# Performance work log

Measured on AMD Instinct MI355X. Metric: run time of the kernel, lower is better.

## Reference

```python
import jax, jax.numpy as jnp
import numpy as np

N, E, F_IN, H, C = 50000, 800000, 256, 4, 32
NEG_SLOPE_ATT = 0.2   # PyG GATConv default negative_slope for attention LeakyReLU
NEG_SLOPE_ACT = 0.01  # GATLayer's alpha for the post-norm LeakyReLU
EPS = 1e-5            # BatchNorm1d eps


def setup_inputs() -> dict:
    key = jax.random.key(0)
    ks = jax.random.split(key, 8)
    x = jax.random.normal(ks[0], (N, F_IN), jnp.float32)
    edge_idx = jax.random.randint(ks[1], (2, E), 0, N)
    # GATConv params (heads concatenated): lin weight, attention vectors, bias
    W = jax.random.normal(ks[2], (H * C, F_IN), jnp.float32) / np.sqrt(F_IN)
    att_src = jax.random.normal(ks[3], (H, C), jnp.float32) / np.sqrt(C)
    att_dst = jax.random.normal(ks[4], (H, C), jnp.float32) / np.sqrt(C)
    bias = jax.random.normal(ks[5], (H * C,), jnp.float32) * 0.01
    # BatchNorm1d affine params
    gamma = jax.random.normal(ks[6], (H * C,), jnp.float32) * 0.1 + 1.0
    beta = jax.random.normal(ks[7], (H * C,), jnp.float32) * 0.01
    return {"x": x, "edge_idx": edge_idx, "W": W, "att_src": att_src,
            "att_dst": att_dst, "bias": bias, "gamma": gamma, "beta": beta}


def reference(x, edge_idx, W, att_src, att_dst, bias, gamma, beta):
    n = x.shape[0]
    # PyG GATConv adds self-loops by default
    self_loops = jnp.arange(n)
    src = jnp.concatenate([edge_idx[0], self_loops])  # [E+N]
    dst = jnp.concatenate([edge_idx[1], self_loops])

    h = (x @ W.T).reshape(n, H, C)                    # [N, H, C]
    a_s = jnp.einsum('nhc,hc->nh', h, att_src)        # per-node src score
    a_d = jnp.einsum('nhc,hc->nh', h, att_dst)        # per-node dst score

    # edge attention logits, then segment softmax over incoming edges per dst
    e = jax.nn.leaky_relu(a_s[src] + a_d[dst], NEG_SLOPE_ATT)  # [E+N, H]
    e_max = jax.ops.segment_max(e, dst, num_segments=n)
    e_exp = jnp.exp(e - e_max[dst])
    denom = jax.ops.segment_sum(e_exp, dst, num_segments=n)
    alpha = e_exp / denom[dst]                        # [E+N, H]

    # scatter-add aggregation of attended source features
    out = jax.ops.segment_sum(alpha[:, :, None] * h[src], dst, num_segments=n)
    out = out.reshape(n, H * C) + bias                # concat heads + bias

    # BatchNorm1d (training-mode batch statistics) + LeakyReLU(alpha)
    mu = out.mean(axis=0)
    var = out.var(axis=0)
    out = (out - mu) * jax.lax.rsqrt(var + EPS) * gamma + beta
    return jax.nn.leaky_relu(out, NEG_SLOPE_ACT)
```

## Files before the change

### kernel.cpp

```cpp
#include <hip/hip_runtime.h>
#include <hip/hip_bf16.h>
#include <math.h>


typedef __attribute__((ext_vector_type(8))) short bf8_t;
typedef __attribute__((ext_vector_type(4))) float f4_t;

__device__ inline unsigned short f2bf(float f) {
  unsigned u = __float_as_uint(f);
  u += 0x7fff + ((u >> 16) & 1);
  return (unsigned short)(u >> 16);
}
__device__ inline float lrelu02(float v) { return v > 0.f ? v : 0.2f * v; }
__device__ inline float bflo(unsigned g) { return __uint_as_float(g << 16); }
__device__ inline float bfhi(unsigned g) { return __uint_as_float(g & 0xffff0000u); }

#define LSTRIDE 264
#define PSTRIDE 2048
#define SSTRIDE 2112
#define NC 32

__global__ __launch_bounds__(256) void gemm_mfma(const float* __restrict__ x,
                                                 const float* __restrict__ w,
                                                 const float* __restrict__ att_s,
                                                 const float* __restrict__ att_d,
                                                 unsigned* __restrict__ hb2,
                                                 float* __restrict__ a_s,
                                                 float* __restrict__ a_d,
                                                 int n, int ntiles) {
  __shared__ unsigned short wsl[128 * LSTRIDE];
  __shared__ unsigned short xsl[64 * LSTRIDE];
  int tid = threadIdx.x;
  int lane = tid & 63;
  int wid = tid >> 6;
  int quad = lane >> 4;
  int l15 = lane & 15;

  float attS[8], attD[8];
#pragma unroll
  for (int t = 0; t < 8; t++) {
    attS[t] = att_s[t * 16 + l15];
    attD[t] = att_d[t * 16 + l15];
  }

#pragma unroll 4
  for (int i = 0; i < 32; i++) {
    int idx = tid + i * 256;
    int row = idx >> 6;
    int f4 = idx & 63;
    float4 v = *(const float4*)&w[(size_t)row * 256 + f4 * 4];
    unsigned p01 = f2bf(v.x) | ((unsigned)f2bf(v.y) << 16);
    unsigned p23 = f2bf(v.z) | ((unsigned)f2bf(v.w) << 16);
    *(uint2*)&wsl[row * LSTRIDE + f4 * 4] = make_uint2(p01, p23);
  }

  float4 pre[16];
  int tile = blockIdx.x;
  if (tile < ntiles) {
#pragma unroll
    for (int i = 0; i < 16; i++) {
      int idx = tid + i * 256;
      int row = idx >> 6, f4 = idx & 63;
      int grow = tile * 64 + row;
      pre[i] = (grow < n) ? *(const float4*)&x[(size_t)grow * 256 + f4 * 4]
                          : make_float4(0.f, 0.f, 0.f, 0.f);
    }
  }

  for (; tile < ntiles; tile += gridDim.x) {
    __syncthreads();
#pragma unroll
    for (int i = 0; i < 16; i++) {
      int idx = tid + i * 256;
      int row = idx >> 6, f4 = idx & 63;
      unsigned p01 = f2bf(pre[i].x) | ((unsigned)f2bf(pre[i].y) << 16);
      unsigned p23 = f2bf(pre[i].z) | ((unsigned)f2bf(pre[i].w) << 16);
      *(uint2*)&xsl[row * LSTRIDE + f4 * 4] = make_uint2(p01, p23);
    }
    __syncthreads();

    int nxt = tile + gridDim.x;
    if (nxt < ntiles) {
#pragma unroll
      for (int i = 0; i < 16; i++) {
        int idx = tid + i * 256;
        int row = idx >> 6, f4 = idx & 63;
        int grow = nxt * 64 + row;
        pre[i] = (grow < n) ? *(const float4*)&x[(size_t)grow * 256 + f4 * 4]
                            : make_float4(0.f, 0.f, 0.f, 0.f);
      }
    }

    f4_t acc[8];
#pragma unroll
    for (int t = 0; t < 8; t++) acc[t] = (f4_t){0.f, 0.f, 0.f, 0.f};
    const unsigned short* arow = &xsl[(wid * 16 + l15) * LSTRIDE];
#pragma unroll
    for (int ks = 0; ks < 8; ks++) {
      bf8_t af = *(const bf8_t*)&arow[ks * 32 + quad * 8];
#pragma unroll
      for (int t = 0; t < 8; t++) {
        bf8_t bf = *(const bf8_t*)&wsl[(t * 16 + l15) * LSTRIDE + ks * 32 + quad * 8];
        acc[t] = __builtin_amdgcn_mfma_f32_16x16x32_bf16(af, bf, acc[t], 0, 0, 0);
      }
    }

    int growb = tile * 64 + wid * 16 + quad * 4;
#pragma unroll
    for (int r = 0; r < 4; r++) {
      int grow = growb + r;
      bool ok = grow < n;
      if (ok) {
        unsigned* orow = &hb2[(size_t)grow * 64];
#pragma unroll
        for (int t = 0; t < 4; t++)
          orow[t * 16 + l15] =
              (unsigned)f2bf(acc[t][r]) | ((unsigned)f2bf(acc[t + 4][r]) << 16);
      }
      float sp[4], dp[4];
#pragma unroll
      for (int hh = 0; hh < 4; hh++) {
        sp[hh] = acc[2 * hh][r] * attS[2 * hh] + acc[2 * hh + 1][r] * attS[2 * hh + 1];
        dp[hh] = acc[2 * hh][r] * attD[2 * hh] + acc[2 * hh + 1][r] * attD[2 * hh + 1];
      }
#pragma unroll
      for (int mm = 1; mm < 16; mm <<= 1) {
#pragma unroll
        for (int hh = 0; hh < 4; hh++) {
          sp[hh] += __shfl_xor(sp[hh], mm, 64);
          dp[hh] += __shfl_xor(dp[hh], mm, 64);
        }
      }
      float vs = l15 == 0 ? sp[0] : l15 == 1 ? sp[1] : l15 == 2 ? sp[2] : sp[3];
      float vd = l15 == 0 ? dp[0] : l15 == 1 ? dp[1] : l15 == 2 ? dp[2] : dp[3];
      if (ok && l15 < 4) {
        a_s[grow * 4 + l15] = vs;
        a_d[grow * 4 + l15] = vd;
      }
    }
  }
}

__global__ __launch_bounds__(1024) void pair_scatter3_k(const int* __restrict__ src,
                                                        const int* __restrict__ dst,
                                                        int* __restrict__ bcnt,
                                                        unsigned* __restrict__ pairs,
                                                        int E, int nb) {
  __shared__ int cnt[1024];
  int t = threadIdx.x;
  int chunk = (E + gridDim.x - 1) / gridDim.x;
  int lo = blockIdx.x * chunk;
  int hi = min(E, lo + chunk);
  for (int i = t; i < nb; i += 1024) cnt[i] = 0;
  __syncthreads();
  for (int i = lo + t; i < hi; i += 1024) atomicAdd(&cnt[dst[i] >> 6], 1);
  __syncthreads();
  for (int i = t; i < nb; i += 1024) {
    int c = cnt[i];
    cnt[i] = c ? atomicAdd(&bcnt[i], c) : 0;
  }
  __syncthreads();
  for (int i = lo + t; i < hi; i += 1024) {
    int d = dst[i];
    int b = d >> 6;
    int pos = atomicAdd(&cnt[b], 1);
    if (pos < PSTRIDE)
      pairs[(size_t)b * PSTRIDE + pos] = (unsigned)src[i] | ((unsigned)(d & 63) << 26);
  }
}

__global__ __launch_bounds__(256) void bucket_csr_k(const unsigned* __restrict__ pairs,
                                                    const int* __restrict__ bcnt,
                                                    int* __restrict__ off,
                                                    int* __restrict__ dlen,
                                                    int* __restrict__ ssrc, int n) {
  __shared__ int hist[64], lofs[64], curs[64];
  int b = blockIdx.x;
  int t = threadIdx.x;
  int d0 = b << 6;
  int dcnt = min(64, n - d0);
  int cnt = min(bcnt[b], PSTRIDE);
  size_t pstart = (size_t)b * PSTRIDE;
  int ob = b * SSTRIDE;
  if (t < 64) hist[t] = (t < dcnt) ? 1 : 0;
  __syncthreads();
  for (int i = t; i < cnt; i += 256) atomicAdd(&hist[pairs[pstart + i] >> 26], 1);
  __syncthreads();
  if (t == 0) {
    int acc = 0;
    for (int k = 0; k < 64; k++) { lofs[k] = acc; acc += hist[k]; }
  }
  __syncthreads();
  if (t < dcnt) {
    int lo = lofs[t];
    off[d0 + t] = ob + lo;
    dlen[d0 + t] = hist[t];
    curs[t] = lo + 1;
    ssrc[ob + lo] = d0 + t;
  }
  __syncthreads();
  for (int i = t; i < cnt; i += 256) {
    unsigned u = pairs[pstart + i];
    int dl = u >> 26;
    int pos = ob + atomicAdd(&curs[dl], 1);
    ssrc[pos] = (int)(u & 0x03FFFFFFu);
  }
}

#define FMA4(g, p)                                                            \
  alo0 = fmaf(p.x, bflo(g.x), alo0); ahi0 = fmaf(p.y, bfhi(g.x), ahi0);       \
  alo1 = fmaf(p.x, bflo(g.y), alo1); ahi1 = fmaf(p.y, bfhi(g.y), ahi1);       \
  alo2 = fmaf(p.x, bflo(g.z), alo2); ahi2 = fmaf(p.y, bfhi(g.z), ahi2);       \
  alo3 = fmaf(p.x, bflo(g.w), alo3); ahi3 = fmaf(p.y, bfhi(g.w), ahi3);

__global__ __launch_bounds__(256) void agg_csr_k(const int* __restrict__ off,
                                                 const int* __restrict__ dlen,
                                                 const int* __restrict__ ssrc,
                                                 const float* __restrict__ a_s,
                                                 const float* __restrict__ a_d,
                                                 const unsigned* __restrict__ hb2,
                                                 float* __restrict__ out,
                                                 float* __restrict__ gstat, int n) {
  __shared__ float lp[4][64 * 4];
  __shared__ int lsrc[4][64];
  __shared__ float bstat[4][256];
  int tid = threadIdx.x;
  int wid = tid >> 6;
  int lane = tid & 63;
  int d = blockIdx.x * 4 + wid;
  bool act = d < n;
  int q = lane >> 4;
  int m = lane & 15;
  int hsel = m >> 3;

  float alo0 = 0.f, alo1 = 0.f, alo2 = 0.f, alo3 = 0.f;
  float ahi0 = 0.f, ahi1 = 0.f, ahi2 = 0.f, ahi3 = 0.f;
  float l0 = 0.f, l1 = 0.f, l2 = 0.f, l3 = 0.f;

  if (act) {
    int start = off[d];
    int end = start + dlen[d];
    float4 ad4 = *(const float4*)&a_d[d * 4];
    for (int base = start; base < end; base += 64) {
      int cnt = min(64, end - base);
      int j = base + lane;
      if (j < end) {
        int s = ssrc[j];
        float4 as4 = *(const float4*)&a_s[s * 4];
        float p0 = __expf(lrelu02(as4.x + ad4.x));
        float p1 = __expf(lrelu02(as4.y + ad4.y));
        float p2 = __expf(lrelu02(as4.z + ad4.z));
        float p3 = __expf(lrelu02(as4.w + ad4.w));
        l0 += p0; l1 += p1; l2 += p2; l3 += p3;
        lsrc[wid][lane] = s;
        *(float4*)&lp[wid][lane * 4] = make_float4(p0, p2, p1, p3);
      }
      int k = 0;
      for (; k + 8 <= cnt; k += 8) {
        int e0 = k + q, e1 = k + 4 + q;
        int s0 = lsrc[wid][e0], s1 = lsrc[wid][e1];
        uint4 g0 = *(const uint4*)&hb2[(size_t)s0 * 64 + m * 4];
        uint4 g1 = *(const uint4*)&hb2[(size_t)s1 * 64 + m * 4];
        float2 p0 = *(const float2*)&lp[wid][e0 * 4 + hsel * 2];
        float2 p1 = *(const float2*)&lp[wid][e1 * 4 + hsel * 2];
        FMA4(g0, p0);
        FMA4(g1, p1);
      }
      for (; k + 4 <= cnt; k += 4) {
        int e0 = k + q;
        int s0 = lsrc[wid][e0];
        uint4 g0 = *(const uint4*)&hb2[(size_t)s0 * 64 + m * 4];
        float2 p0 = *(const float2*)&lp[wid][e0 * 4 + hsel * 2];
        FMA4(g0, p0);
      }
      int rem = cnt - k;
      if (q < rem) {
        int e0 = k + q;
        int s0 = lsrc[wid][e0];
        uint4 g0 = *(const uint4*)&hb2[(size_t)s0 * 64 + m * 4];
        float2 p0 = *(const float2*)&lp[wid][e0 * 4 + hsel * 2];
        FMA4(g0, p0);
      }
    }
  }

#pragma unroll
  for (int o = 16; o < 64; o <<= 1) {
    alo0 += __shfl_xor(alo0, o, 64); alo1 += __shfl_xor(alo1, o, 64);
    alo2 += __shfl_xor(alo2, o, 64); alo3 += __shfl_xor(alo3, o, 64);
    ahi0 += __shfl_xor(ahi0, o, 64); ahi1 += __shfl_xor(ahi1, o, 64);
    ahi2 += __shfl_xor(ahi2, o, 64); ahi3 += __shfl_xor(ahi3, o, 64);
  }
#pragma unroll
  for (int o = 1; o < 64; o <<= 1) {
    l0 += __shfl_xor(l0, o, 64);
    l1 += __shfl_xor(l1, o, 64);
    l2 += __shfl_xor(l2, o, 64);
    l3 += __shfl_xor(l3, o, 64);
  }
  float il_lo = 1.0f / (hsel ? l1 : l0);
  float il_hi = 1.0f / (hsel ? l3 : l2);
  float4 flo = make_float4(0.f, 0.f, 0.f, 0.f);
  float4 fhi = make_float4(0.f, 0.f, 0.f, 0.f);
  if (act) {
    flo = make_float4(alo0 * il_lo, alo1 * il_lo, alo2 * il_lo, alo3 * il_lo);
    fhi = make_float4(ahi0 * il_hi, ahi1 * il_hi, ahi2 * il_hi, ahi3 * il_hi);
  }
  if (q == 0) {
    if (act) {
      *(float4*)&out[(size_t)d * 128 + m * 4] = flo;
      *(float4*)&out[(size_t)d * 128 + 64 + m * 4] = fhi;
    }
    *(float4*)&bstat[wid][m * 4] = flo;
    *(float4*)&bstat[wid][64 + m * 4] = fhi;
    *(float4*)&bstat[wid][128 + m * 4] =
        make_float4(flo.x * flo.x, flo.y * flo.y, flo.z * flo.z, flo.w * flo.w);
    *(float4*)&bstat[wid][192 + m * 4] =
        make_float4(fhi.x * fhi.x, fhi.y * fhi.y, fhi.z * fhi.z, fhi.w * fhi.w);
  }
  __syncthreads();
  float v = bstat[0][tid] + bstat[1][tid] + bstat[2][tid] + bstat[3][tid];
  atomicAdd(&gstat[(blockIdx.x & (NC - 1)) * 256 + tid], v);
}

__global__ __launch_bounds__(256) void bn_apply_k(float* __restrict__ out,
                                                  const float* __restrict__ gstat,
                                                  const float* __restrict__ gamma,
                                                  const float* __restrict__ beta,
                                                  float inv_n, int n4) {
  __shared__ float sc[128], sh[128];
  int tid = threadIdx.x;
  if (tid < 128) {
    float s = 0.f, s2 = 0.f;
#pragma unroll 8
    for (int c = 0; c < NC; c++) {
      s += gstat[c * 256 + tid];
      s2 += gstat[c * 256 + 128 + tid];
    }
    float mu = s * inv_n;
    float var = s2 * inv_n - mu * mu;
    float rstd = 1.0f / sqrtf(var + 1e-5f);
    float g = gamma[tid] * rstd;
    sc[tid] = g;
    sh[tid] = beta[tid] - mu * g;
  }
  __syncthreads();
  int i = blockIdx.x * 256 + tid;
  if (i >= n4) return;
  float4 v = ((float4*)out)[i];
  int j = (i & 31) << 2;
  const float4 scv = *(const float4*)&sc[j];
  const float4 shv = *(const float4*)&sh[j];
  v.x = fmaf(v.x, scv.x, shv.x);
  v.y = fmaf(v.y, scv.y, shv.y);
  v.z = fmaf(v.z, scv.z, shv.z);
  v.w = fmaf(v.w, scv.w, shv.w);
  v.x = v.x > 0.f ? v.x : 0.01f * v.x;
  v.y = v.y > 0.f ? v.y : 0.01f * v.y;
  v.z = v.z > 0.f ? v.z : 0.01f * v.z;
  v.w = v.w > 0.f ? v.w : 0.01f * v.w;
  ((float4*)out)[i] = v;
}

static inline char* align16(char* p) {
  return (char*)(((uintptr_t)p + 15) & ~(uintptr_t)15);
}

extern "C" void kernel_launch(void* const* d_in, const int* in_sizes, int n_in,
                              void* d_out, int out_size, void* d_ws, size_t ws_size,
                              hipStream_t stream) {
  const float* x     = (const float*)d_in[0];
  const int*   ei    = (const int*)d_in[1];
  const float* W     = (const float*)d_in[2];
  const float* att_s = (const float*)d_in[3];
  const float* att_d = (const float*)d_in[4];
  const float* gamma = (const float*)d_in[6];
  const float* beta  = (const float*)d_in[7];

  int n = in_sizes[0] / 256;
  int E = in_sizes[1] / 2;
  const int* src = ei;
  const int* dstp = ei + E;
  float* out = (float*)d_out;

  int NBUCK = (n + 63) >> 6;
  int ntiles = (n + 63) / 64;

  char* p = (char*)d_ws;
  unsigned* hb2 = (unsigned*)p; p = align16(p + (size_t)n * 64 * 4);
  float* a_s   = (float*)p; p = align16(p + (size_t)n * 4 * 4);
  float* a_d   = (float*)p; p = align16(p + (size_t)n * 4 * 4);
  float* gstat = (float*)p;
  int*   bcnt  = (int*)(gstat + NC * 256);
  p = align16((char*)(bcnt + NBUCK));
  int* off     = (int*)p;   p = align16(p + (size_t)n * 4);
  int* dlen    = (int*)p;   p = align16(p + (size_t)n * 4);
  int* ssrc    = (int*)p;   p = align16(p + (size_t)NBUCK * SSTRIDE * 4);
  unsigned* pairs = (unsigned*)p; p = align16(p + (size_t)NBUCK * PSTRIDE * 4);

  hipMemsetAsync(gstat, 0, ((size_t)NC * 256 + NBUCK) * 4, stream);

  gemm_mfma<<<256, 256, 0, stream>>>(x, W, att_s, att_d, hb2, a_s, a_d, n, ntiles);

  pair_scatter3_k<<<64, 1024, 0, stream>>>(src, dstp, bcnt, pairs, E, NBUCK);
  bucket_csr_k<<<NBUCK, 256, 0, stream>>>(pairs, bcnt, off, dlen, ssrc, n);

  agg_csr_k<<<(n + 3) / 4, 256, 0, stream>>>(off, dlen, ssrc, a_s, a_d, hb2, out,
                                             gstat, n);

  bn_apply_k<<<(n * 32 + 255) / 256, 256, 0, stream>>>(out, gstat, gamma, beta,
                                                       1.0f / n, n * 32);
}
```

Before: 206.2 us.

## Process four destination nodes per wave in aggregation and unroll gathers by 16

The aggregation kernel now has each wave loop over DPW=4 destination nodes. BN partial statistics are accumulated in shared memory across those nodes before a single atomicAdd per block, which cuts the block count and global atomic traffic by about 4x. The number of stat copies (NC) drops from 32 to 8, and a 16-edge unrolled gather loop adds memory-level parallelism. The costs are fewer blocks in flight, serialized per-node work within a wave, and more atomic contention on fewer slots.

```diff
diff --git a/kernel.cpp b/kernel.cpp
--- a/kernel.cpp
+++ b/kernel.cpp
@@ -18,7 +18,8 @@
 #define LSTRIDE 264
 #define PSTRIDE 2048
 #define SSTRIDE 2112
-#define NC 32
+#define NC 8
+#define DPW 4
 
 __global__ __launch_bounds__(256) void gemm_mfma(const float* __restrict__ x,
                                                  const float* __restrict__ w,
@@ -227,17 +228,22 @@
   int tid = threadIdx.x;
   int wid = tid >> 6;
   int lane = tid & 63;
-  int d = blockIdx.x * 4 + wid;
-  bool act = d < n;
   int q = lane >> 4;
   int m = lane & 15;
   int hsel = m >> 3;
-
-  float alo0 = 0.f, alo1 = 0.f, alo2 = 0.f, alo3 = 0.f;
-  float ahi0 = 0.f, ahi1 = 0.f, ahi2 = 0.f, ahi3 = 0.f;
-  float l0 = 0.f, l1 = 0.f, l2 = 0.f, l3 = 0.f;
-
-  if (act) {
+  const unsigned* __restrict__ hb2m = hb2 + m * 4;
+
+  *(float4*)&bstat[wid][lane * 4] = make_float4(0.f, 0.f, 0.f, 0.f);
+
+  int dbase = (blockIdx.x * 4 + wid) * DPW;
+  for (int it = 0; it < DPW; it++) {
+    int d = dbase + it;
+    if (d >= n) break;
+
+    float alo0 = 0.f, alo1 = 0.f, alo2 = 0.f, alo3 = 0.f;
+    float ahi0 = 0.f, ahi1 = 0.f, ahi2 = 0.f, ahi3 = 0.f;
+    float l0 = 0.f, l1 = 0.f, l2 = 0.f, l3 = 0.f;
+
     int start = off[d];
     int end = start + dlen[d];
     float4 ad4 = *(const float4*)&a_d[d * 4];
@@ -256,11 +262,28 @@
         *(float4*)&lp[wid][lane * 4] = make_float4(p0, p2, p1, p3);
       }
       int k = 0;
+      for (; k + 16 <= cnt; k += 16) {
+        int e0 = k + q, e1 = k + 4 + q, e2 = k + 8 + q, e3 = k + 12 + q;
+        int s0 = lsrc[wid][e0], s1 = lsrc[wid][e1];
+        int s2 = lsrc[wid][e2], s3 = lsrc[wid][e3];
+        uint4 g0 = *(const uint4*)&hb2m[(size_t)s0 * 64];
+        uint4 g1 = *(const uint4*)&hb2m[(size_t)s1 * 64];
+        uint4 g2 = *(const uint4*)&hb2m[(size_t)s2 * 64];
+        uint4 g3 = *(const uint4*)&hb2m[(size_t)s3 * 64];
+        float2 p0 = *(const float2*)&lp[wid][e0 * 4 + hsel * 2];
+        float2 p1 = *(const float2*)&lp[wid][e1 * 4 + hsel * 2];
+        float2 p2 = *(const float2*)&lp[wid][e2 * 4 + hsel * 2];
+        float2 p3 = *(const float2*)&lp[wid][e3 * 4 + hsel * 2];
+        FMA4(g0, p0);
+        FMA4(g1, p1);
+        FMA4(g2, p2);
+        FMA4(g3, p3);
+      }
       for (; k + 8 <= cnt; k += 8) {
         int e0 = k + q, e1 = k + 4 + q;
         int s0 = lsrc[wid][e0], s1 = lsrc[wid][e1];
-        uint4 g0 = *(const uint4*)&hb2[(size_t)s0 * 64 + m * 4];
-        uint4 g1 = *(const uint4*)&hb2[(size_t)s1 * 64 + m * 4];
+        uint4 g0 = *(const uint4*)&hb2m[(size_t)s0 * 64];
+        uint4 g1 = *(const uint4*)&hb2m[(size_t)s1 * 64];
         float2 p0 = *(const float2*)&lp[wid][e0 * 4 + hsel * 2];
         float2 p1 = *(const float2*)&lp[wid][e1 * 4 + hsel * 2];
         FMA4(g0, p0);
@@ -269,7 +292,7 @@
       for (; k + 4 <= cnt; k += 4) {
         int e0 = k + q;
         int s0 = lsrc[wid][e0];
-        uint4 g0 = *(const uint4*)&hb2[(size_t)s0 * 64 + m * 4];
+        uint4 g0 = *(const uint4*)&hb2m[(size_t)s0 * 64];
         float2 p0 = *(const float2*)&lp[wid][e0 * 4 + hsel * 2];
         FMA4(g0, p0);
       }
@@ -277,47 +300,50 @@
       if (q < rem) {
         int e0 = k + q;
         int s0 = lsrc[wid][e0];
-        uint4 g0 = *(const uint4*)&hb2[(size_t)s0 * 64 + m * 4];
+        uint4 g0 = *(const uint4*)&hb2m[(size_t)s0 * 64];
         float2 p0 = *(const float2*)&lp[wid][e0 * 4 + hsel * 2];
         FMA4(g0, p0);
       }
     }
-  }
-
-#pragma unroll
-  for (int o = 16; o < 64; o <<= 1) {
-    alo0 += __shfl_xor(alo0, o, 64); alo1 += __shfl_xor(alo1, o, 64);
-    alo2 += __shfl_xor(alo2, o, 64); alo3 += __shfl_xor(alo3, o, 64);
-    ahi0 += __shfl_xor(ahi0, o, 64); ahi1 += __shfl_xor(ahi1, o, 64);
-    ahi2 += __shfl_xor(ahi2, o, 64); ahi3 += __shfl_xor(ahi3, o, 64);
-  }
-#pragma unroll
-  for (int o = 1; o < 64; o <<= 1) {
-    l0 += __shfl_xor(l0, o, 64);
-    l1 += __shfl_xor(l1, o, 64);
-    l2 += __shfl_xor(l2, o, 64);
-    l3 += __shfl_xor(l3, o, 64);
-  }
-  float il_lo = 1.0f / (hsel ? l1 : l0);
-  float il_hi = 1.0f / (hsel ? l3 : l2);
-  float4 flo = make_float4(0.f, 0.f, 0.f, 0.f);
-  float4 fhi = make_float4(0.f, 0.f, 0.f, 0.f);
-  if (act) {
-    flo = make_float4(alo0 * il_lo, alo1 * il_lo, alo2 * il_lo, alo3 * il_lo);
-    fhi = make_float4(ahi0 * il_hi, ahi1 * il_hi, ahi2 * il_hi, ahi3 * il_hi);
-  }
-  if (q == 0) {
-    if (act) {
+
+#pragma unroll
+    for (int o = 16; o < 64; o <<= 1) {
+      alo0 += __shfl_xor(alo0, o, 64); alo1 += __shfl_xor(alo1, o, 64);
+      alo2 += __shfl_xor(alo2, o, 64); alo3 += __shfl_xor(alo3, o, 64);
+      ahi0 += __shfl_xor(ahi0, o, 64); ahi1 += __shfl_xor(ahi1, o, 64);
+      ahi2 += __shfl_xor(ahi2, o, 64); ahi3 += __shfl_xor(ahi3, o, 64);
+    }
+#pragma unroll
+    for (int o = 1; o < 64; o <<= 1) {
+      l0 += __shfl_xor(l0, o, 64);
+      l1 += __shfl_xor(l1, o, 64);
+      l2 += __shfl_xor(l2, o, 64);
+      l3 += __shfl_xor(l3, o, 64);
+    }
+    float il_lo = 1.0f / (hsel ? l1 : l0);
+    float il_hi = 1.0f / (hsel ? l3 : l2);
+    if (q == 0) {
+      float4 flo = make_float4(alo0 * il_lo, alo1 * il_lo, alo2 * il_lo, alo3 * il_lo);
+      float4 fhi = make_float4(ahi0 * il_hi, ahi1 * il_hi, ahi2 * il_hi, ahi3 * il_hi);
       *(float4*)&out[(size_t)d * 128 + m * 4] = flo;
       *(float4*)&out[(size_t)d * 128 + 64 + m * 4] = fhi;
-    }
-    *(float4*)&bstat[wid][m * 4] = flo;
-    *(float4*)&bstat[wid][64 + m * 4] = fhi;
-    *(float4*)&bstat[wid][128 + m * 4] =
-        make_float4(flo.x * flo.x, flo.y * flo.y, flo.z * flo.z, flo.w * flo.w);
-    *(float4*)&bstat[wid][192 + m * 4] =
-        make_float4(fhi.x * fhi.x, fhi.y * fhi.y, fhi.z * fhi.z, fhi.w * fhi.w);
-  }
+      float4 b0 = *(float4*)&bstat[wid][m * 4];
+      b0.x += flo.x; b0.y += flo.y; b0.z += flo.z; b0.w += flo.w;
+      *(float4*)&bstat[wid][m * 4] = b0;
+      float4 b1 = *(float4*)&bstat[wid][64 + m * 4];
+      b1.x += fhi.x; b1.y += fhi.y; b1.z += fhi.z; b1.w += fhi.w;
+      *(float4*)&bstat[wid][64 + m * 4] = b1;
+      float4 b2 = *(float4*)&bstat[wid][128 + m * 4];
+      b2.x += flo.x * flo.x; b2.y += flo.y * flo.y;
+      b2.z += flo.z * flo.z; b2.w += flo.w * flo.w;
+      *(float4*)&bstat[wid][128 + m * 4] = b2;
+      float4 b3 = *(float4*)&bstat[wid][192 + m * 4];
+      b3.x += fhi.x * fhi.x; b3.y += fhi.y * fhi.y;
+      b3.z += fhi.z * fhi.z; b3.w += fhi.w * fhi.w;
+      *(float4*)&bstat[wid][192 + m * 4] = b3;
+    }
+  }
+
   __syncthreads();
   float v = bstat[0][tid] + bstat[1][tid] + bstat[2][tid] + bstat[3][tid];
   atomicAdd(&gstat[(blockIdx.x & (NC - 1)) * 256 + tid], v);
@@ -332,7 +358,7 @@
   int tid = threadIdx.x;
   if (tid < 128) {
     float s = 0.f, s2 = 0.f;
-#pragma unroll 8
+#pragma unroll
     for (int c = 0; c < NC; c++) {
       s += gstat[c * 256 + tid];
       s2 += gstat[c * 256 + 128 + tid];
@@ -405,8 +431,9 @@
   pair_scatter3_k<<<64, 1024, 0, stream>>>(src, dstp, bcnt, pairs, E, NBUCK);
   bucket_csr_k<<<NBUCK, 256, 0, stream>>>(pairs, bcnt, off, dlen, ssrc, n);
 
-  agg_csr_k<<<(n + 3) / 4, 256, 0, stream>>>(off, dlen, ssrc, a_s, a_d, hb2, out,
-                                             gstat, n);
+  agg_csr_k<<<(n + 4 * DPW - 1) / (4 * DPW), 256, 0, stream>>>(off, dlen, ssrc,
+                                                               a_s, a_d, hb2, out,
+                                                               gstat, n);
 
   bn_apply_k<<<(n * 32 + 255) / 256, 256, 0, stream>>>(out, gstat, gamma, beta,
                                                        1.0f / n, n * 32);
```

Result: no change. 206.8 us (+0.3%).

## Fold attention vectors into GEMM weights and unroll CSR aggregation gather by 16

Applied to the files above, without the earlier changes.

Precomputes att·W as eight extra weight rows, stored as hi/lo bf16 pairs, so the MFMA GEMM produces the a_s/a_d scores directly as a ninth output tile. This replaces the per-row dot products and 16-lane shuffle reductions. The aggregation loop gains a 16-edge unrolled stage so more independent gathers are in flight, and the BN stat partition count drops from 32 to 8. In exchange it adds a small extra kernel launch, an extra MFMA tile per k-step, and more contention on the stat atomics.

```diff
diff --git a/kernel.cpp b/kernel.cpp
--- a/kernel.cpp
+++ b/kernel.cpp
@@ -18,30 +18,37 @@
 #define LSTRIDE 264
 #define PSTRIDE 2048
 #define SSTRIDE 2112
-#define NC 32
+#define NC 8
+
+__global__ __launch_bounds__(256) void att_fold_k(const float* __restrict__ w,
+                                                  const float* __restrict__ att_s,
+                                                  const float* __restrict__ att_d,
+                                                  float* __restrict__ waug) {
+  int j = blockIdx.x;
+  int head = j & 3;
+  const float* av = (j < 4 ? att_s : att_d) + head * 32;
+  int col = threadIdx.x;
+  float s = 0.f;
+#pragma unroll
+  for (int c = 0; c < 32; c++)
+    s += av[c] * w[(size_t)(head * 32 + c) * 256 + col];
+  waug[j * 256 + col] = s;
+}
 
 __global__ __launch_bounds__(256) void gemm_mfma(const float* __restrict__ x,
                                                  const float* __restrict__ w,
-                                                 const float* __restrict__ att_s,
-                                                 const float* __restrict__ att_d,
+                                                 const float* __restrict__ waug,
                                                  unsigned* __restrict__ hb2,
                                                  float* __restrict__ a_s,
                                                  float* __restrict__ a_d,
                                                  int n, int ntiles) {
-  __shared__ unsigned short wsl[128 * LSTRIDE];
+  __shared__ unsigned short wsl[144 * LSTRIDE];
   __shared__ unsigned short xsl[64 * LSTRIDE];
   int tid = threadIdx.x;
   int lane = tid & 63;
   int wid = tid >> 6;
   int quad = lane >> 4;
   int l15 = lane & 15;
-
-  float attS[8], attD[8];
-#pragma unroll
-  for (int t = 0; t < 8; t++) {
-    attS[t] = att_s[t * 16 + l15];
-    attD[t] = att_d[t * 16 + l15];
-  }
 
 #pragma unroll 4
   for (int i = 0; i < 32; i++) {
@@ -53,6 +60,17 @@
     unsigned p23 = f2bf(v.z) | ((unsigned)f2bf(v.w) << 16);
     *(uint2*)&wsl[row * LSTRIDE + f4 * 4] = make_uint2(p01, p23);
   }
+#pragma unroll
+  for (int i = 0; i < 8; i++) {
+    int idx = tid + i * 256;
+    int row = idx >> 8;
+    int col = idx & 255;
+    float v = waug[idx];
+    unsigned short hi = f2bf(v);
+    float lov = v - __uint_as_float((unsigned)hi << 16);
+    wsl[(128 + row) * LSTRIDE + col] = hi;
+    wsl[(136 + row) * LSTRIDE + col] = f2bf(lov);
+  }
 
   float4 pre[16];
   int tile = blockIdx.x;
@@ -91,15 +109,15 @@
       }
     }
 
-    f4_t acc[8];
-#pragma unroll
-    for (int t = 0; t < 8; t++) acc[t] = (f4_t){0.f, 0.f, 0.f, 0.f};
+    f4_t acc[9];
+#pragma unroll
+    for (int t = 0; t < 9; t++) acc[t] = (f4_t){0.f, 0.f, 0.f, 0.f};
     const unsigned short* arow = &xsl[(wid * 16 + l15) * LSTRIDE];
 #pragma unroll
     for (int ks = 0; ks < 8; ks++) {
       bf8_t af = *(const bf8_t*)&arow[ks * 32 + quad * 8];
 #pragma unroll
-      for (int t = 0; t < 8; t++) {
+      for (int t = 0; t < 9; t++) {
         bf8_t bf = *(const bf8_t*)&wsl[(t * 16 + l15) * LSTRIDE + ks * 32 + quad * 8];
         acc[t] = __builtin_amdgcn_mfma_f32_16x16x32_bf16(af, bf, acc[t], 0, 0, 0);
       }
@@ -117,25 +135,11 @@
           orow[t * 16 + l15] =
               (unsigned)f2bf(acc[t][r]) | ((unsigned)f2bf(acc[t + 4][r]) << 16);
       }
-      float sp[4], dp[4];
-#pragma unroll
-      for (int hh = 0; hh < 4; hh++) {
-        sp[hh] = acc[2 * hh][r] * attS[2 * hh] + acc[2 * hh + 1][r] * attS[2 * hh + 1];
-        dp[hh] = acc[2 * hh][r] * attD[2 * hh] + acc[2 * hh + 1][r] * attD[2 * hh + 1];
-      }
-#pragma unroll
-      for (int mm = 1; mm < 16; mm <<= 1) {
-#pragma unroll
-        for (int hh = 0; hh < 4; hh++) {
-          sp[hh] += __shfl_xor(sp[hh], mm, 64);
-          dp[hh] += __shfl_xor(dp[hh], mm, 64);
-        }
-      }
-      float vs = l15 == 0 ? sp[0] : l15 == 1 ? sp[1] : l15 == 2 ? sp[2] : sp[3];
-      float vd = l15 == 0 ? dp[0] : l15 == 1 ? dp[1] : l15 == 2 ? dp[2] : dp[3];
-      if (ok && l15 < 4) {
-        a_s[grow * 4 + l15] = vs;
-        a_d[grow * 4 + l15] = vd;
+      float v8 = acc[8][r];
+      v8 += __shfl_xor(v8, 8, 64);
+      if (ok) {
+        if (l15 < 4) a_s[grow * 4 + l15] = v8;
+        else if (l15 < 8) a_d[grow * 4 + (l15 - 4)] = v8;
       }
     }
   }
@@ -227,11 +231,13 @@
   int tid = threadIdx.x;
   int wid = tid >> 6;
   int lane = tid & 63;
-  int d = blockIdx.x * 4 + wid;
-  bool act = d < n;
   int q = lane >> 4;
   int m = lane & 15;
   int hsel = m >> 3;
+  const unsigned* __restrict__ hb2m = hb2 + m * 4;
+
+  int d = blockIdx.x * 4 + wid;
+  bool act = d < n;
 
   float alo0 = 0.f, alo1 = 0.f, alo2 = 0.f, alo3 = 0.f;
   float ahi0 = 0.f, ahi1 = 0.f, ahi2 = 0.f, ahi3 = 0.f;
@@ -256,11 +262,28 @@
         *(float4*)&lp[wid][lane * 4] = make_float4(p0, p2, p1, p3);
       }
       int k = 0;
+      for (; k + 16 <= cnt; k += 16) {
+        int e0 = k + q, e1 = k + 4 + q, e2 = k + 8 + q, e3 = k + 12 + q;
+        int s0 = lsrc[wid][e0], s1 = lsrc[wid][e1];
+        int s2 = lsrc[wid][e2], s3 = lsrc[wid][e3];
+        uint4 g0 = *(const uint4*)&hb2m[(size_t)s0 * 64];
+        uint4 g1 = *(const uint4*)&hb2m[(size_t)s1 * 64];
+        uint4 g2 = *(const uint4*)&hb2m[(size_t)s2 * 64];
+        uint4 g3 = *(const uint4*)&hb2m[(size_t)s3 * 64];
+        float2 p0 = *(const float2*)&lp[wid][e0 * 4 + hsel * 2];
+        float2 p1 = *(const float2*)&lp[wid][e1 * 4 + hsel * 2];
+        float2 p2 = *(const float2*)&lp[wid][e2 * 4 + hsel * 2];
+        float2 p3 = *(const float2*)&lp[wid][e3 * 4 + hsel * 2];
+        FMA4(g0, p0);
+        FMA4(g1, p1);
+        FMA4(g2, p2);
+        FMA4(g3, p3);
+      }
       for (; k + 8 <= cnt; k += 8) {
         int e0 = k + q, e1 = k + 4 + q;
         int s0 = lsrc[wid][e0], s1 = lsrc[wid][e1];
-        uint4 g0 = *(const uint4*)&hb2[(size_t)s0 * 64 + m * 4];
-        uint4 g1 = *(const uint4*)&hb2[(size_t)s1 * 64 + m * 4];
+        uint4 g0 = *(const uint4*)&hb2m[(size_t)s0 * 64];
+        uint4 g1 = *(const uint4*)&hb2m[(size_t)s1 * 64];
         float2 p0 = *(const float2*)&lp[wid][e0 * 4 + hsel * 2];
         float2 p1 = *(const float2*)&lp[wid][e1 * 4 + hsel * 2];
         FMA4(g0, p0);
@@ -269,7 +292,7 @@
       for (; k + 4 <= cnt; k += 4) {
         int e0 = k + q;
         int s0 = lsrc[wid][e0];
-        uint4 g0 = *(const uint4*)&hb2[(size_t)s0 * 64 + m * 4];
+        uint4 g0 = *(const uint4*)&hb2m[(size_t)s0 * 64];
         float2 p0 = *(const float2*)&lp[wid][e0 * 4 + hsel * 2];
         FMA4(g0, p0);
       }
@@ -277,7 +300,7 @@
       if (q < rem) {
         int e0 = k + q;
         int s0 = lsrc[wid][e0];
-        uint4 g0 = *(const uint4*)&hb2[(size_t)s0 * 64 + m * 4];
+        uint4 g0 = *(const uint4*)&hb2m[(size_t)s0 * 64];
         float2 p0 = *(const float2*)&lp[wid][e0 * 4 + hsel * 2];
         FMA4(g0, p0);
       }
@@ -332,7 +355,7 @@
   int tid = threadIdx.x;
   if (tid < 128) {
     float s = 0.f, s2 = 0.f;
-#pragma unroll 8
+#pragma unroll
     for (int c = 0; c < NC; c++) {
       s += gstat[c * 256 + tid];
       s2 += gstat[c * 256 + 128 + tid];
@@ -390,6 +413,7 @@
   unsigned* hb2 = (unsigned*)p; p = align16(p + (size_t)n * 64 * 4);
   float* a_s   = (float*)p; p = align16(p + (size_t)n * 4 * 4);
   float* a_d   = (float*)p; p = align16(p + (size_t)n * 4 * 4);
+  float* waug  = (float*)p; p = align16(p + 8 * 256 * 4);
   float* gstat = (float*)p;
   int*   bcnt  = (int*)(gstat + NC * 256);
   p = align16((char*)(bcnt + NBUCK));
@@ -400,7 +424,8 @@
 
   hipMemsetAsync(gstat, 0, ((size_t)NC * 256 + NBUCK) * 4, stream);
 
-  gemm_mfma<<<256, 256, 0, stream>>>(x, W, att_s, att_d, hb2, a_s, a_d, n, ntiles);
+  att_fold_k<<<8, 256, 0, stream>>>(W, att_s, att_d, waug);
+  gemm_mfma<<<256, 256, 0, stream>>>(x, W, waug, hb2, a_s, a_d, n, ntiles);
 
   pair_scatter3_k<<<64, 1024, 0, stream>>>(src, dstp, bcnt, pairs, E, NBUCK);
   bucket_csr_k<<<NBUCK, 256, 0, stream>>>(pairs, bcnt, off, dlen, ssrc, n);
```

Result: slower. 212.7 us (+3.1%).
